# Optimization experiments

Hardware: AMD Instinct MI355X
Metric: run time of the kernel (lower is better)

Reference implementation:

```python
import jax, jax.numpy as jnp
import numpy as np


def setup_inputs() -> dict:
    key = jax.random.key(0)
    k1, k2 = jax.random.split(key)
    B, N, M, D = 8, 8192, 8192, 3
    pred_seq = jax.random.normal(k1, (B, N, D), dtype=jnp.float32)
    tgt_output = jax.random.normal(k2, (B, M, D), dtype=jnp.float32)
    return {"pred_seq": pred_seq, "tgt_output": tgt_output}


def reference(pred_seq, tgt_output):
    # Euclidean pairwise distances [B, N, M] (== torch.cdist with p=2).
    # The torch module computes both cdist(pred,tgt) and cdist(tgt,pred);
    # they are transposes, so we compute one matrix and min over both axes.
    sq_p = jnp.sum(pred_seq * pred_seq, axis=-1)      # [B, N]
    sq_t = jnp.sum(tgt_output * tgt_output, axis=-1)  # [B, M]
    cross = jnp.einsum('bnd,bmd->bnm', pred_seq, tgt_output)  # [B, N, M]
    d2 = sq_p[:, :, None] + sq_t[:, None, :] - 2.0 * cross
    d = jnp.sqrt(jnp.maximum(d2, 0.0))
    min_pred_to_true = jnp.min(d, axis=2)   # [B, N]
    min_true_to_pred = jnp.min(d, axis=1)   # [B, M]
    chamfer = (jnp.mean(min_pred_to_true, axis=1) + jnp.mean(min_true_to_pred, axis=1)) / 2.0
    return chamfer  # [B]
```

## Files before the change

kernel.cpp:

```cpp
#include <hip/hip_runtime.h>
#include <math.h>

#define BB 8
#define NPTS 8192
#define NSIDE (BB * NPTS)

#define BLOCK 256
#define RROWS 8
#define QTILE (BLOCK * RROWS)
#define NQT (NPTS / QTILE)
#define TGB 2
#define NTC (NPTS / (64 * TGB))

__device__ __forceinline__ int enc_key(float v) {
    int b = __float_as_int(v);
    return b >= 0 ? b : (b ^ 0x7fffffff);
}
__device__ __forceinline__ float dec_key(int k) {
    int b = k >= 0 ? k : (k ^ 0x7fffffff);
    return __int_as_float(b);
}

__global__ __launch_bounds__(BLOCK) void chamfer_rot(
        const float* __restrict__ pred, const float* __restrict__ tgt,
        int* __restrict__ rk, int* __restrict__ ck) {
    const int b = blockIdx.z;
    const int qt = blockIdx.y;
    const int tc = blockIdx.x;
    const int t = threadIdx.x;
    const int lane = t & 63;

    float nx[RROWS], ny[RROWS], nz[RROWS], wq[RROWS], rmin[RROWS];
    const float* qp = pred + (size_t)b * NPTS * 3;
    #pragma unroll
    for (int r = 0; r < RROWS; ++r) {
        int qi = qt * QTILE + r * BLOCK + t;
        float x = qp[qi * 3 + 0], y = qp[qi * 3 + 1], z = qp[qi * 3 + 2];
        nx[r] = -2.0f * x;
        ny[r] = -2.0f * y;
        nz[r] = -2.0f * z;
        wq[r] = fmaf(x, x, fmaf(y, y, z * z));
        rmin[r] = INFINITY;
    }

    const int rot = ((lane + 1) & 63) * 4;
    const float* tp = tgt + (size_t)b * NPTS * 3;

    #pragma unroll
    for (int g = 0; g < TGB; ++g) {
        const int tbase = (tc * TGB + g) * 64;
        const int ti = tbase + lane;
        float tx = tp[ti * 3 + 0], ty = tp[ti * 3 + 1], tz = tp[ti * 3 + 2];
        float tw = fmaf(tx, tx, fmaf(ty, ty, tz * tz));
        float cmin = INFINITY;

        #pragma unroll 4
        for (int s = 0; s < 64; ++s) {
            float a[RROWS];
            #pragma unroll
            for (int r = 0; r < RROWS; ++r) {
                float v = fmaf(nx[r], tx, tw + wq[r]);
                v = fmaf(ny[r], ty, v);
                v = fmaf(nz[r], tz, v);
                a[r] = v;
                rmin[r] = fminf(rmin[r], v);
            }
            float m1 = fminf(fminf(a[0], a[1]), fminf(a[2], a[3]));
            float m2 = fminf(fminf(a[4], a[5]), fminf(a[6], a[7]));
            cmin = fminf(cmin, fminf(m1, m2));
            tx = __int_as_float(__builtin_amdgcn_ds_bpermute(rot, __float_as_int(tx)));
            ty = __int_as_float(__builtin_amdgcn_ds_bpermute(rot, __float_as_int(ty)));
            tz = __int_as_float(__builtin_amdgcn_ds_bpermute(rot, __float_as_int(tz)));
            tw = __int_as_float(__builtin_amdgcn_ds_bpermute(rot, __float_as_int(tw)));
            cmin = __int_as_float(__builtin_amdgcn_ds_bpermute(rot, __float_as_int(cmin)));
        }
        atomicMin(&ck[(size_t)b * NPTS + ti], enc_key(cmin));
    }

    #pragma unroll
    for (int r = 0; r < RROWS; ++r) {
        int qi = qt * QTILE + r * BLOCK + t;
        atomicMin(&rk[(size_t)b * NPTS + qi], enc_key(rmin[r]));
    }
}

#define FSLICE 32
__global__ __launch_bounds__(BLOCK) void chamfer_finalize(
        const int* __restrict__ rk, const int* __restrict__ ck,
        float* __restrict__ out) {
    const int b = blockIdx.x / FSLICE;
    const int s = blockIdx.x % FSLICE;
    const int t = threadIdx.x;
    const int span = NPTS / FSLICE;
    const int i = b * NPTS + s * span + t;
    float v = 0.0f;
    if (t < span)
        v = sqrtf(fmaxf(dec_key(rk[i]), 0.0f)) + sqrtf(fmaxf(dec_key(ck[i]), 0.0f));
    __shared__ float red[BLOCK];
    red[t] = v * (0.5f / (float)NPTS);
    __syncthreads();
    for (int off = BLOCK / 2; off > 0; off >>= 1) {
        if (t < off) red[t] += red[t + off];
        __syncthreads();
    }
    if (t == 0) atomicAdd(&out[b], red[0]);
}

extern "C" void kernel_launch(void* const* d_in, const int* in_sizes, int n_in,
                              void* d_out, int out_size, void* d_ws, size_t ws_size,
                              hipStream_t stream) {
    const float* pred = (const float*)d_in[0];
    const float* tgtp = (const float*)d_in[1];
    float* out = (float*)d_out;

    int* rk = (int*)d_ws;
    int* ck = rk + NSIDE;

    hipMemsetAsync(rk, 0x7F, (size_t)2 * NSIDE * sizeof(int), stream);
    hipMemsetAsync(out, 0, (size_t)BB * sizeof(float), stream);

    chamfer_rot<<<dim3(NTC, NQT, BB), BLOCK, 0, stream>>>(pred, tgtp, rk, ck);

    chamfer_finalize<<<BB * FSLICE, BLOCK, 0, stream>>>(rk, ck, out);
}
```

Measured before the change: 130.2 us.

## Compute squared distances with bf16 MFMA using split hi/lo operand packing

Adds a pack kernel that writes each point as a 16-wide bf16 vector with hi/lo split terms, norms and ones. A 32x32x16 bf16 MFMA then yields the full squared distance matrix tile, replacing the scalar FMA loop and its ds_bpermute rotation. Row minima use lane shuffles and column minima go through shared-memory atomics before global atomics. The pack kernel also replaces the memsets. The split bf16 representation trades exact fp32 accuracy for matrix-core throughput, and it adds a pack pass plus many LDS atomics per tile.

Result: faster. 124.8 us (-4.2%).

```diff
diff --git a/kernel.cpp b/kernel.cpp
--- a/kernel.cpp
+++ b/kernel.cpp
@@ -6,11 +6,15 @@
 #define NSIDE (BB * NPTS)
 
 #define BLOCK 256
-#define RROWS 8
-#define QTILE (BLOCK * RROWS)
-#define NQT (NPTS / QTILE)
-#define TGB 2
-#define NTC (NPTS / (64 * TGB))
+#define WARPS 4
+#define ROWSB (32 * WARPS)
+#define TCHUNK 2048
+#define NTILES (TCHUNK / 32)
+
+#define INF_KEY 0x7F7F7F7F
+
+typedef short bf16x8 __attribute__((ext_vector_type(8)));
+typedef float f32x16 __attribute__((ext_vector_type(16)));
 
 __device__ __forceinline__ int enc_key(float v) {
     int b = __float_as_int(v);
@@ -21,67 +25,135 @@
     return __int_as_float(b);
 }
 
-__global__ __launch_bounds__(BLOCK) void chamfer_rot(
+__device__ __forceinline__ unsigned short f2bf(float f) {
+    unsigned u = __float_as_uint(f);
+    return (unsigned short)((u + 0x7FFFu + ((u >> 16) & 1u)) >> 16);
+}
+__device__ __forceinline__ float bfhi(float f, unsigned short* bits) {
+    unsigned short h = f2bf(f);
+    *bits = h;
+    return __uint_as_float(((unsigned)h) << 16);
+}
+
+__global__ __launch_bounds__(BLOCK) void chamfer_pack(
         const float* __restrict__ pred, const float* __restrict__ tgt,
+        unsigned short* __restrict__ pA, unsigned short* __restrict__ pB,
+        int* __restrict__ rk, int* __restrict__ ck, float* __restrict__ out) {
+    int i = blockIdx.x * BLOCK + threadIdx.x;
+    const unsigned short one = 0x3F80;
+
+    {
+        float x = pred[(size_t)i * 3 + 0], y = pred[(size_t)i * 3 + 1],
+              z = pred[(size_t)i * 3 + 2];
+        float wq = fmaf(x, x, fmaf(y, y, z * z));
+        float ax = -2.0f * x, ay = -2.0f * y, az = -2.0f * z;
+        unsigned short hx, hy, hz, hw;
+        float fhx = bfhi(ax, &hx), fhy = bfhi(ay, &hy), fhz = bfhi(az, &hz);
+        float fhw = bfhi(wq, &hw);
+        unsigned short lx = f2bf(ax - fhx), ly = f2bf(ay - fhy),
+                       lz = f2bf(az - fhz), lw = f2bf(wq - fhw);
+        unsigned short s[16] = {hx, hx, lx, hy, hy, ly, hz, hz, lz,
+                                hw, lw, one, one, 0, 0, 0};
+        uint4* dst = (uint4*)(pA + (size_t)i * 16);
+        uint4 w0 = {(unsigned)s[0] | ((unsigned)s[1] << 16),
+                    (unsigned)s[2] | ((unsigned)s[3] << 16),
+                    (unsigned)s[4] | ((unsigned)s[5] << 16),
+                    (unsigned)s[6] | ((unsigned)s[7] << 16)};
+        uint4 w1 = {(unsigned)s[8] | ((unsigned)s[9] << 16),
+                    (unsigned)s[10] | ((unsigned)s[11] << 16),
+                    (unsigned)s[12] | ((unsigned)s[13] << 16),
+                    (unsigned)s[14] | ((unsigned)s[15] << 16)};
+        dst[0] = w0; dst[1] = w1;
+    }
+    {
+        float x = tgt[(size_t)i * 3 + 0], y = tgt[(size_t)i * 3 + 1],
+              z = tgt[(size_t)i * 3 + 2];
+        float tw = fmaf(x, x, fmaf(y, y, z * z));
+        unsigned short hx, hy, hz, hw;
+        float fhx = bfhi(x, &hx), fhy = bfhi(y, &hy), fhz = bfhi(z, &hz);
+        float fhw = bfhi(tw, &hw);
+        unsigned short lx = f2bf(x - fhx), ly = f2bf(y - fhy),
+                       lz = f2bf(z - fhz), lw = f2bf(tw - fhw);
+        unsigned short s[16] = {hx, lx, hx, hy, ly, hy, hz, lz, hz,
+                                one, one, hw, lw, 0, 0, 0};
+        uint4* dst = (uint4*)(pB + (size_t)i * 16);
+        uint4 w0 = {(unsigned)s[0] | ((unsigned)s[1] << 16),
+                    (unsigned)s[2] | ((unsigned)s[3] << 16),
+                    (unsigned)s[4] | ((unsigned)s[5] << 16),
+                    (unsigned)s[6] | ((unsigned)s[7] << 16)};
+        uint4 w1 = {(unsigned)s[8] | ((unsigned)s[9] << 16),
+                    (unsigned)s[10] | ((unsigned)s[11] << 16),
+                    (unsigned)s[12] | ((unsigned)s[13] << 16),
+                    (unsigned)s[14] | ((unsigned)s[15] << 16)};
+        dst[0] = w0; dst[1] = w1;
+    }
+    rk[i] = INF_KEY;
+    ck[i] = INF_KEY;
+    if (i < BB) out[i] = 0.0f;
+}
+
+__global__ __launch_bounds__(BLOCK) void chamfer_mfma(
+        const unsigned short* __restrict__ pA, const unsigned short* __restrict__ pB,
         int* __restrict__ rk, int* __restrict__ ck) {
     const int b = blockIdx.z;
-    const int qt = blockIdx.y;
-    const int tc = blockIdx.x;
-    const int t = threadIdx.x;
-    const int lane = t & 63;
+    const int tb0 = blockIdx.x * TCHUNK;
+    const int rb0 = blockIdx.y * ROWSB;
+    const int wave = threadIdx.x >> 6;
+    const int lane = threadIdx.x & 63;
+    const int lp = lane & 31;
+    const int kh = lane >> 5;
 
-    float nx[RROWS], ny[RROWS], nz[RROWS], wq[RROWS], rmin[RROWS];
-    const float* qp = pred + (size_t)b * NPTS * 3;
+    __shared__ int colkey[TCHUNK];
+    for (int j = threadIdx.x; j < TCHUNK; j += BLOCK) colkey[j] = INF_KEY;
+    __syncthreads();
+
+    const bf16x8* Ap = (const bf16x8*)pA;
+    const bf16x8* Bp = (const bf16x8*)pB;
+    const bf16x8 afrag = Ap[(size_t)(b * NPTS + rb0 + wave * 32 + lp) * 2 + kh];
+
+    f32x16 zero;
     #pragma unroll
-    for (int r = 0; r < RROWS; ++r) {
-        int qi = qt * QTILE + r * BLOCK + t;
-        float x = qp[qi * 3 + 0], y = qp[qi * 3 + 1], z = qp[qi * 3 + 2];
-        nx[r] = -2.0f * x;
-        ny[r] = -2.0f * y;
-        nz[r] = -2.0f * z;
-        wq[r] = fmaf(x, x, fmaf(y, y, z * z));
-        rmin[r] = INFINITY;
-    }
+    for (int k = 0; k < 16; ++k) zero[k] = 0.0f;
 
-    const int rot = ((lane + 1) & 63) * 4;
-    const float* tp = tgt + (size_t)b * NPTS * 3;
+    float rmin[16];
+    #pragma unroll
+    for (int k = 0; k < 16; ++k) rmin[k] = INFINITY;
 
-    #pragma unroll
-    for (int g = 0; g < TGB; ++g) {
-        const int tbase = (tc * TGB + g) * 64;
-        const int ti = tbase + lane;
-        float tx = tp[ti * 3 + 0], ty = tp[ti * 3 + 1], tz = tp[ti * 3 + 2];
-        float tw = fmaf(tx, tx, fmaf(ty, ty, tz * tz));
-        float cmin = INFINITY;
+    size_t bidx = (size_t)(b * NPTS + tb0 + lp) * 2 + kh;
 
-        #pragma unroll 4
-        for (int s = 0; s < 64; ++s) {
-            float a[RROWS];
-            #pragma unroll
-            for (int r = 0; r < RROWS; ++r) {
-                float v = fmaf(nx[r], tx, tw + wq[r]);
-                v = fmaf(ny[r], ty, v);
-                v = fmaf(nz[r], tz, v);
-                a[r] = v;
-                rmin[r] = fminf(rmin[r], v);
-            }
-            float m1 = fminf(fminf(a[0], a[1]), fminf(a[2], a[3]));
-            float m2 = fminf(fminf(a[4], a[5]), fminf(a[6], a[7]));
-            cmin = fminf(cmin, fminf(m1, m2));
-            tx = __int_as_float(__builtin_amdgcn_ds_bpermute(rot, __float_as_int(tx)));
-            ty = __int_as_float(__builtin_amdgcn_ds_bpermute(rot, __float_as_int(ty)));
-            tz = __int_as_float(__builtin_amdgcn_ds_bpermute(rot, __float_as_int(tz)));
-            tw = __int_as_float(__builtin_amdgcn_ds_bpermute(rot, __float_as_int(tw)));
-            cmin = __int_as_float(__builtin_amdgcn_ds_bpermute(rot, __float_as_int(cmin)));
-        }
-        atomicMin(&ck[(size_t)b * NPTS + ti], enc_key(cmin));
+    #pragma unroll 2
+    for (int tile = 0; tile < NTILES; ++tile) {
+        const bf16x8 bfrag = Bp[bidx];
+        bidx += 64;
+        f32x16 d = __builtin_amdgcn_mfma_f32_32x32x16_bf16(afrag, bfrag, zero, 0, 0, 0);
+        #pragma unroll
+        for (int k = 0; k < 16; ++k) rmin[k] = fminf(rmin[k], d[k]);
+        float c0 = fminf(fminf(d[0], d[1]), fminf(d[2], d[3]));
+        float c1 = fminf(fminf(d[4], d[5]), fminf(d[6], d[7]));
+        float c2 = fminf(fminf(d[8], d[9]), fminf(d[10], d[11]));
+        float c3 = fminf(fminf(d[12], d[13]), fminf(d[14], d[15]));
+        float cp = fminf(fminf(c0, c1), fminf(c2, c3));
+        atomicMin(&colkey[tile * 32 + lp], enc_key(cp));
     }
 
     #pragma unroll
-    for (int r = 0; r < RROWS; ++r) {
-        int qi = qt * QTILE + r * BLOCK + t;
-        atomicMin(&rk[(size_t)b * NPTS + qi], enc_key(rmin[r]));
+    for (int k = 0; k < 16; ++k) {
+        #pragma unroll
+        for (int off = 1; off <= 16; off <<= 1)
+            rmin[k] = fminf(rmin[k], __shfl_xor(rmin[k], off));
     }
+    if (lp == 0) {
+        #pragma unroll
+        for (int k = 0; k < 16; ++k) {
+            int row = (k & 3) + 8 * (k >> 2) + 4 * kh;
+            atomicMin(&rk[(size_t)b * NPTS + rb0 + wave * 32 + row],
+                      enc_key(rmin[k]));
+        }
+    }
+
+    __syncthreads();
+    for (int j = threadIdx.x; j < TCHUNK; j += BLOCK)
+        atomicMin(&ck[(size_t)b * NPTS + tb0 + j], colkey[j]);
 }
 
 #define FSLICE 32
@@ -91,11 +163,9 @@
     const int b = blockIdx.x / FSLICE;
     const int s = blockIdx.x % FSLICE;
     const int t = threadIdx.x;
-    const int span = NPTS / FSLICE;
-    const int i = b * NPTS + s * span + t;
-    float v = 0.0f;
-    if (t < span)
-        v = sqrtf(fmaxf(dec_key(rk[i]), 0.0f)) + sqrtf(fmaxf(dec_key(ck[i]), 0.0f));
+    const int i = b * NPTS + s * (NPTS / FSLICE) + t;
+    float v = sqrtf(fmaxf(dec_key(rk[i]), 0.0f)) +
+              sqrtf(fmaxf(dec_key(ck[i]), 0.0f));
     __shared__ float red[BLOCK];
     red[t] = v * (0.5f / (float)NPTS);
     __syncthreads();
@@ -113,13 +183,16 @@
     const float* tgtp = (const float*)d_in[1];
     float* out = (float*)d_out;
 
-    int* rk = (int*)d_ws;
+    char* ws = (char*)d_ws;
+    unsigned short* pA = (unsigned short*)ws;
+    unsigned short* pB = (unsigned short*)(ws + (size_t)NSIDE * 32);
+    int* rk = (int*)(ws + (size_t)2 * NSIDE * 32);
     int* ck = rk + NSIDE;
 
-    hipMemsetAsync(rk, 0x7F, (size_t)2 * NSIDE * sizeof(int), stream);
-    hipMemsetAsync(out, 0, (size_t)BB * sizeof(float), stream);
+    chamfer_pack<<<NSIDE / BLOCK, BLOCK, 0, stream>>>(pred, tgtp, pA, pB, rk, ck, out);
 
-    chamfer_rot<<<dim3(NTC, NQT, BB), BLOCK, 0, stream>>>(pred, tgtp, rk, ck);
+    chamfer_mfma<<<dim3(NPTS / TCHUNK, NPTS / ROWSB, BB), BLOCK, 0, stream>>>(
+        pA, pB, rk, ck);
 
     chamfer_finalize<<<BB * FSLICE, BLOCK, 0, stream>>>(rk, ck, out);
 }
```
